# Performance work log

Hardware: AMD Instinct MI355X
Metric: run time of the kernel (lower is better)

Reference implementation:

```python
import jax, jax.numpy as jnp
import numpy as np

N, E, D, H, C, TD, MD = 50000, 500000, 128, 2, 64, 32, 64


def setup_inputs() -> dict:
    key = jax.random.key(0)
    ks = jax.random.split(key, 16)
    s = 0.05
    return {
        "x": jax.random.normal(ks[0], (N, D), jnp.float32),
        "edge_index": jax.random.randint(ks[1], (2, E), 0, N, dtype=jnp.int64),
        "edge_time": jax.random.randint(ks[2], (E,), 0, 86400, dtype=jnp.int64),
        "msg": jax.random.normal(ks[3], (E, MD), jnp.float32),
        "Wt": jax.random.normal(ks[4], (1, TD), jnp.float32) * s,
        "bt": jax.random.normal(ks[5], (TD,), jnp.float32) * s,
        "Wq": jax.random.normal(ks[6], (D, H * C), jnp.float32) * s,
        "bq": jax.random.normal(ks[7], (H * C,), jnp.float32) * s,
        "Wk": jax.random.normal(ks[8], (D, H * C), jnp.float32) * s,
        "bk": jax.random.normal(ks[9], (H * C,), jnp.float32) * s,
        "Wv": jax.random.normal(ks[10], (D, H * C), jnp.float32) * s,
        "bv": jax.random.normal(ks[11], (H * C,), jnp.float32) * s,
        "We": jax.random.normal(ks[12], (TD + MD, H * C), jnp.float32) * s,
        "Wskip": jax.random.normal(ks[13], (D, H * C), jnp.float32) * s,
        "bskip": jax.random.normal(ks[14], (H * C,), jnp.float32) * s,
    }


def reference(x, edge_index, edge_time, msg, Wt, bt, Wq, bq, Wk, bk, Wv, bv, We, Wskip, bskip):
    n = x.shape[0]
    src, dst = edge_index[0], edge_index[1]

    # TGN-style time encoding: cos(Linear(t))  -> [E, TD]
    t = edge_time.astype(x.dtype)[:, None]
    rel_t = jnp.cos(t @ Wt + bt)
    edge_attr = jnp.concatenate([rel_t, msg], axis=-1)  # [E, TD+MD]

    # TransformerConv projections, reshaped to [n, H, C] then gathered per edge
    q = (x @ Wq + bq).reshape(n, H, C)[dst]   # [E, H, C]
    k = (x @ Wk + bk).reshape(n, H, C)[src]   # [E, H, C]
    v = (x @ Wv + bv).reshape(n, H, C)[src]   # [E, H, C]
    e = (edge_attr @ We).reshape(-1, H, C)    # [E, H, C]

    k = k + e
    alpha = (q * k).sum(-1) / jnp.sqrt(jnp.asarray(C, x.dtype))  # [E, H]

    # segment softmax over incoming edges of each dst node
    amax = jax.ops.segment_max(alpha, dst, num_segments=n)       # [n, H]
    amax = jnp.where(jnp.isfinite(amax), amax, 0.0)
    ex = jnp.exp(alpha - amax[dst])
    denom = jax.ops.segment_sum(ex, dst, num_segments=n)
    alpha = ex / (denom[dst] + 1e-16)                            # [E, H]

    out_e = (v + e) * alpha[..., None]                           # [E, H, C]
    out = jax.ops.segment_sum(out_e, dst, num_segments=n).reshape(n, H * C)

    # root/skip connection
    out = out + x @ Wskip + bskip
    return out
```

## Files before the change

kernel.cpp:

```cpp
#include <hip/hip_runtime.h>
#include <hip/hip_bf16.h>

#define NN 50000
#define NE 500000
#define DD 128
#define HCC 128
#define TDD 32
#define MDD 64

typedef __hip_bfloat16 bf16;
typedef _Float16 f16;
typedef __attribute__((ext_vector_type(8))) _Float16 f16x8;
typedef __attribute__((ext_vector_type(2))) _Float16 f16x2;
typedef __attribute__((ext_vector_type(4))) float f32x4;

__device__ __forceinline__ float2 bf2x(unsigned u) {
    union { unsigned v; float f; } a, b;
    a.v = u << 16; b.v = u & 0xffff0000u;
    float2 r; r.x = a.f; r.y = b.f; return r;
}

__global__ __launch_bounds__(256) void conv_w_kernel(
    const float* __restrict__ Wq, const float* __restrict__ Wk,
    const float* __restrict__ Wv, const float* __restrict__ Wsk,
    const float* __restrict__ We,
    f16* __restrict__ WTh, f16* __restrict__ Weh, int* __restrict__ cnt)
{
    int idx = blockIdx.x * 256 + threadIdx.x;
    if (idx < 512 * 128) {
        int n = idx >> 7, k = idx & 127;
        int mat = n >> 7, col = n & 127;
        const float* W = (mat == 0) ? Wq : (mat == 1) ? Wk : (mat == 2) ? Wv : Wsk;
        WTh[idx] = (f16)W[k * 128 + col];
    } else if (idx < 512 * 128 + 96 * 128) {
        int i = idx - 512 * 128;
        Weh[i] = (f16)We[i];
    } else if (idx < 512 * 128 + 96 * 128 + NN) {
        cnt[idx - (512 * 128 + 96 * 128)] = 0;
    }
}

__global__ __launch_bounds__(256) void node_proj_kernel(
    const float* __restrict__ x, const f16* __restrict__ WTh,
    const float* __restrict__ bq, const float* __restrict__ bk,
    const float* __restrict__ bv, const float* __restrict__ bsk,
    f16* __restrict__ qh, f16* __restrict__ kh, f16* __restrict__ vh,
    float* __restrict__ outp)
{
    __shared__ f16 xs[64 * 136];
    __shared__ f16 ws[128 * 136];

    const int node0 = blockIdx.x * 64;
    const int g = blockIdx.y;

    for (int i = threadIdx.x; i < 64 * 32; i += 256) {
        int node = i >> 5, koff = (i & 31) * 4;
        int gn = node0 + node;
        f16 o4[4] = { (f16)0.f, (f16)0.f, (f16)0.f, (f16)0.f };
        if (gn < NN) {
            float4 v = *(const float4*)&x[(size_t)gn * DD + koff];
            o4[0] = (f16)v.x; o4[1] = (f16)v.y; o4[2] = (f16)v.z; o4[3] = (f16)v.w;
        }
        *(uint2*)&xs[node * 136 + koff] = *(uint2*)o4;
    }
    const f16* wt = WTh + (size_t)g * 128 * 128;
    for (int i = threadIdx.x; i < 128 * 32; i += 256) {
        int n = i >> 5, koff = (i & 31) * 4;
        *(uint2*)&ws[n * 136 + koff] = *(const uint2*)&wt[n * 128 + koff];
    }
    __syncthreads();

    const int wave = threadIdx.x >> 6;
    const int lane = threadIdx.x & 63;
    const int m0 = wave * 16;
    const int lrow = lane & 15;
    const int lk = (lane >> 4) * 8;

    f32x4 acc[8];
    #pragma unroll
    for (int t = 0; t < 8; t++) acc[t] = (f32x4){0.f, 0.f, 0.f, 0.f};

    #pragma unroll
    for (int kc = 0; kc < 4; kc++) {
        f16x8 a = *(const f16x8*)&xs[(m0 + lrow) * 136 + kc * 32 + lk];
        #pragma unroll
        for (int t = 0; t < 8; t++) {
            f16x8 b = *(const f16x8*)&ws[(t * 16 + lrow) * 136 + kc * 32 + lk];
            acc[t] = __builtin_amdgcn_mfma_f32_16x16x32_f16(a, b, acc[t], 0, 0, 0);
        }
    }

    const float* bias = (g == 0) ? bq : (g == 1) ? bk : (g == 2) ? bv : bsk;
    f16* outh = (g == 0) ? qh : (g == 1) ? kh : vh;

    #pragma unroll 1
    for (int t = 0; t < 8; t++) {
        int col = t * 16 + lrow;
        float bc = bias[col];
        #pragma unroll
        for (int r = 0; r < 4; r++) {
            int node = node0 + m0 + (lane >> 4) * 4 + r;
            if (node < NN) {
                float val = acc[t][r] + bc;
                if (g < 3) outh[(size_t)node * HCC + col] = (f16)val;
                else       outp[(size_t)node * HCC + col] = val;
            }
        }
    }
}

__global__ __launch_bounds__(256) void g_kernel(
    const f16* __restrict__ qh, const f16* __restrict__ Weh,
    bf16* __restrict__ G)
{
    __shared__ f16 qs[64 * 136];
    __shared__ f16 ws[96 * 136];

    const int node0 = blockIdx.x * 64;
    for (int i = threadIdx.x; i < 64 * 32; i += 256) {
        int node = i >> 5, koff = (i & 31) * 4;
        int gn = node0 + node;
        uint2 val = {0u, 0u};
        if (gn < NN) val = *(const uint2*)&qh[(size_t)gn * DD + koff];
        *(uint2*)&qs[node * 136 + koff] = val;
    }
    for (int i = threadIdx.x; i < 96 * 32; i += 256) {
        int j = i >> 5, koff = (i & 31) * 4;
        *(uint2*)&ws[j * 136 + koff] = *(const uint2*)&Weh[j * 128 + koff];
    }
    __syncthreads();

    const int wave = threadIdx.x >> 6;
    const int lane = threadIdx.x & 63;
    const int m0 = wave * 16;
    const int lrow = lane & 15;
    const int lk = (lane >> 4) * 8;

    f16x8 afr[4];
    #pragma unroll
    for (int hk = 0; hk < 4; hk++) {
        int h = hk >> 1, kc = hk & 1;
        afr[hk] = *(const f16x8*)&qs[(m0 + lrow) * 136 + h * 64 + kc * 32 + lk];
    }

    f32x4 acc[12];
    #pragma unroll
    for (int t = 0; t < 12; t++) acc[t] = (f32x4){0.f, 0.f, 0.f, 0.f};

    #pragma unroll
    for (int t = 0; t < 12; t++) {
        int h = (t < 6) ? 0 : 1;
        int jt = (t < 6) ? t : t - 6;
        #pragma unroll
        for (int kc = 0; kc < 2; kc++) {
            f16x8 b = *(const f16x8*)&ws[(jt * 16 + lrow) * 136 + h * 64 + kc * 32 + lk];
            acc[t] = __builtin_amdgcn_mfma_f32_16x16x32_f16(afr[h * 2 + kc], b, acc[t], 0, 0, 0);
        }
    }

    #pragma unroll 1
    for (int t = 0; t < 12; t++) {
        int h = (t < 6) ? 0 : 1;
        int jt = (t < 6) ? t : t - 6;
        int col = h * 96 + jt * 16 + lrow;
        #pragma unroll
        for (int r = 0; r < 4; r++) {
            int node = node0 + m0 + (lane >> 4) * 4 + r;
            if (node < NN) G[(size_t)node * 192 + col] = __float2bfloat16(acc[t][r]);
        }
    }
}

__global__ __launch_bounds__(256) void hist_kernel(
    const int* __restrict__ ei, int* __restrict__ cnt)
{
    int gid = blockIdx.x * 256 + threadIdx.x;
    if (gid < NE) atomicAdd(&cnt[ei[NE + gid]], 1);
}

__global__ __launch_bounds__(256) void scan_a_kernel(
    const int* __restrict__ cnt, int* __restrict__ bsum)
{
    __shared__ int red[256];
    int gid = blockIdx.x * 256 + threadIdx.x;
    red[threadIdx.x] = (gid < NN) ? cnt[gid] : 0;
    __syncthreads();
    for (int off = 128; off > 0; off >>= 1) {
        if (threadIdx.x < off) red[threadIdx.x] += red[threadIdx.x + off];
        __syncthreads();
    }
    if (threadIdx.x == 0) bsum[blockIdx.x] = red[0];
}

__global__ __launch_bounds__(256) void scan_b_kernel(
    const int* __restrict__ bsum, int* __restrict__ boff, int* __restrict__ seg)
{
    __shared__ int s[256];
    int t = threadIdx.x;
    s[t] = (t < 196) ? bsum[t] : 0;
    __syncthreads();
    if (t == 0) {
        int run = 0;
        for (int b = 0; b < 196; b++) { int v = s[b]; s[b] = run; run += v; }
        seg[NN] = NE;
    }
    __syncthreads();
    if (t < 196) boff[t] = s[t];
}

__global__ __launch_bounds__(256) void scan_c_kernel(
    const int* __restrict__ cnt, const int* __restrict__ boff,
    int* __restrict__ seg, int* __restrict__ cur)
{
    __shared__ int s[256];
    int gid = blockIdx.x * 256 + threadIdx.x;
    int v = (gid < NN) ? cnt[gid] : 0;
    s[threadIdx.x] = v;
    __syncthreads();
    for (int off = 1; off < 256; off <<= 1) {
        int t = (threadIdx.x >= off) ? s[threadIdx.x - off] : 0;
        __syncthreads();
        s[threadIdx.x] += t;
        __syncthreads();
    }
    int excl = s[threadIdx.x] - v + boff[blockIdx.x];
    if (gid < NN) { seg[gid] = excl; cur[gid] = excl; }
}

__global__ __launch_bounds__(256) void scatter_kernel(
    const int* __restrict__ ei, const int* __restrict__ et,
    int* __restrict__ cur, int4* __restrict__ epack)
{
    int gid = blockIdx.x * 256 + threadIdx.x;
    if (gid < NE) {
        int d = ei[NE + gid];
        int pos = atomicAdd(&cur[d], 1);
        int4 p;
        p.x = ei[gid];
        p.y = gid;
        p.z = __float_as_int((float)et[gid]);
        p.w = d;
        epack[pos] = p;
    }
}

__global__ __launch_bounds__(256) void agg_kernel(
    const int4* __restrict__ epack, const float* __restrict__ msg,
    const float* __restrict__ Wt, const float* __restrict__ bt,
    const f16* __restrict__ qh, const f16* __restrict__ kh,
    const f16* __restrict__ vh, const bf16* __restrict__ G,
    const int* __restrict__ seg,
    float* __restrict__ Sv, float* __restrict__ dnv,
    float* __restrict__ outp)
{
    __shared__ float wt_s[TDD], bt_s[TDD];
    if (threadIdx.x < TDD) {
        wt_s[threadIdx.x] = Wt[threadIdx.x];
        bt_s[threadIdx.x] = bt[threadIdx.x];
    }
    __syncthreads();

    const int lane = threadIdx.x & 63;
    const int c = lane & 31;
    const int h = lane >> 5;
    const float wtv = wt_s[c];
    const float btv = bt_s[c];
    const int gw = blockIdx.x * 4 + (threadIdx.x >> 6);
    const int NW = gridDim.x * 4;

    for (int n = gw; n < NN; n += NW) {
        const int s0 = seg[n], s1 = seg[n + 1];

        f16x2 q2 = *(const f16x2*)&qh[(size_t)n * DD + 2 * lane];
        const bf16* grow = G + (size_t)n * 192 + 96 * h;
        float Gc  = __bfloat162float(grow[c]);
        float Gm0 = __bfloat162float(grow[32 + 2 * c]);
        float Gm1 = __bfloat162float(grow[33 + 2 * c]);

        float2 acc; acc.x = 0.f; acc.y = 0.f;
        float accd = 0.f, sc = 0.f, sm0 = 0.f, sm1 = 0.f;

        int i = s0;
        #pragma unroll 1
        for (; i + 4 <= s1; i += 4) {
            int4 e[4]; f16x2 k2[4], v2[4]; float2 m[4];
            #pragma unroll
            for (int u = 0; u < 4; u++) e[u] = epack[i + u];
            #pragma unroll
            for (int u = 0; u < 4; u++) {
                int src = e[u].x;
                k2[u] = *(const f16x2*)&kh[(size_t)src * HCC + 2 * lane];
                v2[u] = *(const f16x2*)&vh[(size_t)src * HCC + 2 * lane];
                m[u]  = *(const float2*)&msg[((size_t)e[u].y << 6) + 2 * c];
            }
            #pragma unroll
            for (int u = 0; u < 4; u++) {
                float t = __int_as_float(e[u].z);
                float cs = __cosf(fmaf(t, wtv, btv));
                float p = fmaf(cs, Gc, fmaf(m[u].x, Gm0, m[u].y * Gm1));
#if defined(__has_builtin) && __has_builtin(__builtin_amdgcn_fdot2)
                p = __builtin_amdgcn_fdot2(q2, k2[u], p, false);
#else
                p = fmaf((float)q2[0], (float)k2[u][0], p);
                p = fmaf((float)q2[1], (float)k2[u][1], p);
#endif
                p += __shfl_xor(p, 1);
                p += __shfl_xor(p, 2);
                p += __shfl_xor(p, 4);
                p += __shfl_xor(p, 8);
                p += __shfl_xor(p, 16);
                float ex = __expf(p * 0.125f);
                acc.x = fmaf(ex, (float)v2[u][0], acc.x);
                acc.y = fmaf(ex, (float)v2[u][1], acc.y);
                accd += ex;
                sc  = fmaf(ex, cs, sc);
                sm0 = fmaf(ex, m[u].x, sm0);
                sm1 = fmaf(ex, m[u].y, sm1);
            }
        }
        #pragma unroll 1
        for (; i < s1; i++) {
            int4 e = epack[i];
            int src = e.x;
            f16x2 k2 = *(const f16x2*)&kh[(size_t)src * HCC + 2 * lane];
            f16x2 v2 = *(const f16x2*)&vh[(size_t)src * HCC + 2 * lane];
            float2 m = *(const float2*)&msg[((size_t)e.y << 6) + 2 * c];
            float t = __int_as_float(e.z);
            float cs = __cosf(fmaf(t, wtv, btv));
            float p = fmaf(cs, Gc, fmaf(m.x, Gm0, m.y * Gm1));
#if defined(__has_builtin) && __has_builtin(__builtin_amdgcn_fdot2)
            p = __builtin_amdgcn_fdot2(q2, k2, p, false);
#else
            p = fmaf((float)q2[0], (float)k2[0], p);
            p = fmaf((float)q2[1], (float)k2[1], p);
#endif
            p += __shfl_xor(p, 1);
            p += __shfl_xor(p, 2);
            p += __shfl_xor(p, 4);
            p += __shfl_xor(p, 8);
            p += __shfl_xor(p, 16);
            float ex = __expf(p * 0.125f);
            acc.x = fmaf(ex, (float)v2[0], acc.x);
            acc.y = fmaf(ex, (float)v2[1], acc.y);
            accd += ex;
            sc  = fmaf(ex, cs, sc);
            sm0 = fmaf(ex, m.x, sm0);
            sm1 = fmaf(ex, m.y, sm1);
        }

        float dn = accd + 1e-16f;
        size_t sb = (size_t)n * 192 + 96 * h;
        Sv[sb + c]          = sc;
        Sv[sb + 32 + 2 * c] = sm0;
        Sv[sb + 33 + 2 * c] = sm1;
        if (c == 0) dnv[n * 2 + h] = accd;

        size_t nb = (size_t)n * HCC + 2 * lane;
        float2 sk = *(const float2*)&outp[nb];
        float2 o;
        o.x = acc.x / dn + sk.x;
        o.y = acc.y / dn + sk.y;
        *(float2*)&outp[nb] = o;
    }
}

__global__ __launch_bounds__(256) void epi_kernel(
    const float* __restrict__ Sv, const float* __restrict__ dnv,
    const float* __restrict__ We, float* __restrict__ outp)
{
    __shared__ float st[192 * 36];
    const int node0 = blockIdx.x * 32;
    for (int idx = threadIdx.x; idx < 32 * 192; idx += 256) {
        int n = idx / 192, c = idx - n * 192;
        int node = node0 + n;
        st[c * 36 + n] = (node < NN) ? Sv[(size_t)node * 192 + c] : 0.f;
    }
    __syncthreads();

    const int wave = threadIdx.x >> 6;
    const int lane = threadIdx.x & 63;
    const int nb = wave * 8;
    const int hoff = (lane < 32) ? 0 : 96;
    const float2* We2 = (const float2*)We;

    float a[8][2];
    #pragma unroll
    for (int n = 0; n < 8; n++) { a[n][0] = 0.f; a[n][1] = 0.f; }

    #pragma unroll 8
    for (int j = 0; j < 96; j++) {
        float2 w = We2[j * 64 + lane];
        const float* sr = &st[(hoff + j) * 36 + nb];
        float sv[8];
        *(float4*)&sv[0] = *(const float4*)sr;
        *(float4*)&sv[4] = *(const float4*)(sr + 4);
        #pragma unroll
        for (int n = 0; n < 8; n++) {
            a[n][0] = fmaf(sv[n], w.x, a[n][0]);
            a[n][1] = fmaf(sv[n], w.y, a[n][1]);
        }
    }

    #pragma unroll 1
    for (int n = 0; n < 8; n++) {
        int node = node0 + nb + n;
        if (node >= NN) break;
        float dn = dnv[node * 2 + (lane >> 5)] + 1e-16f;
        size_t b = (size_t)node * HCC + 2 * lane;
        float2 o = *(const float2*)&outp[b];
        o.x += a[n][0] / dn;
        o.y += a[n][1] / dn;
        *(float2*)&outp[b] = o;
    }
}

extern "C" void kernel_launch(void* const* d_in, const int* in_sizes, int n_in,
                              void* d_out, int out_size, void* d_ws, size_t ws_size,
                              hipStream_t stream) {
    const float* x   = (const float*)d_in[0];
    const int* ei    = (const int*)d_in[1];
    const int* et    = (const int*)d_in[2];
    const float* msg = (const float*)d_in[3];
    const float* Wt  = (const float*)d_in[4];
    const float* bt  = (const float*)d_in[5];
    const float* Wq  = (const float*)d_in[6];
    const float* bq  = (const float*)d_in[7];
    const float* Wk  = (const float*)d_in[8];
    const float* bk  = (const float*)d_in[9];
    const float* Wv  = (const float*)d_in[10];
    const float* bv  = (const float*)d_in[11];
    const float* We  = (const float*)d_in[12];
    const float* Wsk = (const float*)d_in[13];
    const float* bsk = (const float*)d_in[14];

    const size_t nf = (size_t)NN * HCC;
    f16* qh      = (f16*)d_ws;
    f16* kh      = qh + nf;
    f16* vh      = kh + nf;
    f16* WTh     = vh + nf;
    f16* Weh     = WTh + 512 * 128;
    bf16* G      = (bf16*)(Weh + 96 * 128);
    float* Sv    = (float*)(G + (size_t)NN * 192);
    float* dnv   = Sv + (size_t)NN * 192;
    int4* epack  = (int4*)(dnv + (size_t)NN * 2);
    int* cnt     = (int*)(epack + NE);
    int* seg     = cnt + NN;
    int* cur     = seg + NN + 1;
    int* bsum    = cur + NN;
    int* boff    = bsum + 256;
    size_t need  = (size_t)((char*)(boff + 256) - (char*)d_ws);
    if (ws_size < need) return;

    float* outp = (float*)d_out;

    conv_w_kernel<<<(512 * 128 + 96 * 128 + NN + 255) / 256, 256, 0, stream>>>(
        Wq, Wk, Wv, Wsk, We, WTh, Weh, cnt);
    dim3 npgrid((NN + 63) / 64, 4);
    node_proj_kernel<<<npgrid, 256, 0, stream>>>(
        x, WTh, bq, bk, bv, bsk, qh, kh, vh, outp);
    g_kernel<<<(NN + 63) / 64, 256, 0, stream>>>(qh, Weh, G);
    hist_kernel<<<(NE + 255) / 256, 256, 0, stream>>>(ei, cnt);
    scan_a_kernel<<<196, 256, 0, stream>>>(cnt, bsum);
    scan_b_kernel<<<1, 256, 0, stream>>>(bsum, boff, seg);
    scan_c_kernel<<<196, 256, 0, stream>>>(cnt, boff, seg, cur);
    scatter_kernel<<<(NE + 255) / 256, 256, 0, stream>>>(ei, et, cur, epack);
    agg_kernel<<<3125, 256, 0, stream>>>(
        epack, msg, Wt, bt, qh, kh, vh, G, seg, Sv, dnv, outp);
    epi_kernel<<<(NN + 31) / 32, 256, 0, stream>>>(Sv, dnv, We, outp);
}
```

Measured before the change: 539.0 us.

## Interleave K/V per node and process two edges per wave in aggregation

Node projection now writes K and V into one interleaved buffer (4 K values then 4 V values per 8-element group), so each edge gathers K and V with a single 16-byte load. The aggregation kernel splits each wave into two 32-lane halves that handle alternate edges, with each lane covering 4 channels, and the halves are combined with cross-half shuffles at the end. The aim is fewer, wider gather loads and fewer shuffle reduction steps per edge. The tail path uses a predicated edge body that recomputes a dummy edge, and the final combination adds shuffle overhead per node.

```diff
diff --git a/kernel.cpp b/kernel.cpp
--- a/kernel.cpp
+++ b/kernel.cpp
@@ -19,6 +19,16 @@
     a.v = u << 16; b.v = u & 0xffff0000u;
     float2 r; r.x = a.f; r.y = b.f; return r;
 }
+
+#if defined(__has_builtin) && __has_builtin(__builtin_amdgcn_fdot2)
+#define FDOT2(a, b, acc) __builtin_amdgcn_fdot2((a), (b), (acc), false)
+#else
+__device__ __forceinline__ float fdot2_sw(f16x2 a, f16x2 b, float acc) {
+    acc = fmaf((float)a[0], (float)b[0], acc);
+    return fmaf((float)a[1], (float)b[1], acc);
+}
+#define FDOT2(a, b, acc) fdot2_sw((a), (b), (acc))
+#endif
 
 __global__ __launch_bounds__(256) void conv_w_kernel(
     const float* __restrict__ Wq, const float* __restrict__ Wk,
@@ -44,7 +54,7 @@
     const float* __restrict__ x, const f16* __restrict__ WTh,
     const float* __restrict__ bq, const float* __restrict__ bk,
     const float* __restrict__ bv, const float* __restrict__ bsk,
-    f16* __restrict__ qh, f16* __restrict__ kh, f16* __restrict__ vh,
+    f16* __restrict__ qh, f16* __restrict__ kvh,
     float* __restrict__ outp)
 {
     __shared__ f16 xs[64 * 136];
@@ -91,7 +101,6 @@
     }
 
     const float* bias = (g == 0) ? bq : (g == 1) ? bk : (g == 2) ? bv : bsk;
-    f16* outh = (g == 0) ? qh : (g == 1) ? kh : vh;
 
     #pragma unroll 1
     for (int t = 0; t < 8; t++) {
@@ -102,8 +111,12 @@
             int node = node0 + m0 + (lane >> 4) * 4 + r;
             if (node < NN) {
                 float val = acc[t][r] + bc;
-                if (g < 3) outh[(size_t)node * HCC + col] = (f16)val;
-                else       outp[(size_t)node * HCC + col] = val;
+                if (g == 0)      qh[(size_t)node * DD + col] = (f16)val;
+                else if (g == 3) outp[(size_t)node * HCC + col] = val;
+                else {
+                    int off = 8 * (col >> 2) + (col & 3) + ((g == 2) ? 4 : 0);
+                    kvh[(size_t)node * 256 + off] = (f16)val;
+                }
             }
         }
     }
@@ -247,120 +260,117 @@
 __global__ __launch_bounds__(256) void agg_kernel(
     const int4* __restrict__ epack, const float* __restrict__ msg,
     const float* __restrict__ Wt, const float* __restrict__ bt,
-    const f16* __restrict__ qh, const f16* __restrict__ kh,
-    const f16* __restrict__ vh, const bf16* __restrict__ G,
-    const int* __restrict__ seg,
+    const f16* __restrict__ qh, const f16* __restrict__ kvh,
+    const bf16* __restrict__ G, const int* __restrict__ seg,
     float* __restrict__ Sv, float* __restrict__ dnv,
     float* __restrict__ outp)
 {
-    __shared__ float wt_s[TDD], bt_s[TDD];
-    if (threadIdx.x < TDD) {
-        wt_s[threadIdx.x] = Wt[threadIdx.x];
-        bt_s[threadIdx.x] = bt[threadIdx.x];
-    }
-    __syncthreads();
-
     const int lane = threadIdx.x & 63;
-    const int c = lane & 31;
-    const int h = lane >> 5;
-    const float wtv = wt_s[c];
-    const float btv = bt_s[c];
+    const int l31 = lane & 31;
+    const int hl = (lane >> 4) & 1;
+    const int c = lane & 15;
+    const int halfid = lane >> 5;
+
+    const float wt0 = Wt[2 * c], wt1 = Wt[2 * c + 1];
+    const float bt0 = bt[2 * c], bt1 = bt[2 * c + 1];
+
     const int gw = blockIdx.x * 4 + (threadIdx.x >> 6);
     const int NW = gridDim.x * 4;
 
+    union QU { uint2 u; f16x2 h[2]; };
+    union KVU { uint4 u4; f16x2 h[4]; };
+
     for (int n = gw; n < NN; n += NW) {
         const int s0 = seg[n], s1 = seg[n + 1];
 
-        f16x2 q2 = *(const f16x2*)&qh[(size_t)n * DD + 2 * lane];
-        const bf16* grow = G + (size_t)n * 192 + 96 * h;
-        float Gc  = __bfloat162float(grow[c]);
-        float Gm0 = __bfloat162float(grow[32 + 2 * c]);
-        float Gm1 = __bfloat162float(grow[33 + 2 * c]);
-
-        float2 acc; acc.x = 0.f; acc.y = 0.f;
-        float accd = 0.f, sc = 0.f, sm0 = 0.f, sm1 = 0.f;
-
-        int i = s0;
-        #pragma unroll 1
-        for (; i + 4 <= s1; i += 4) {
-            int4 e[4]; f16x2 k2[4], v2[4]; float2 m[4];
-            #pragma unroll
-            for (int u = 0; u < 4; u++) e[u] = epack[i + u];
-            #pragma unroll
-            for (int u = 0; u < 4; u++) {
-                int src = e[u].x;
-                k2[u] = *(const f16x2*)&kh[(size_t)src * HCC + 2 * lane];
-                v2[u] = *(const f16x2*)&vh[(size_t)src * HCC + 2 * lane];
-                m[u]  = *(const float2*)&msg[((size_t)e[u].y << 6) + 2 * c];
-            }
-            #pragma unroll
-            for (int u = 0; u < 4; u++) {
-                float t = __int_as_float(e[u].z);
-                float cs = __cosf(fmaf(t, wtv, btv));
-                float p = fmaf(cs, Gc, fmaf(m[u].x, Gm0, m[u].y * Gm1));
-#if defined(__has_builtin) && __has_builtin(__builtin_amdgcn_fdot2)
-                p = __builtin_amdgcn_fdot2(q2, k2[u], p, false);
-#else
-                p = fmaf((float)q2[0], (float)k2[u][0], p);
-                p = fmaf((float)q2[1], (float)k2[u][1], p);
-#endif
-                p += __shfl_xor(p, 1);
-                p += __shfl_xor(p, 2);
-                p += __shfl_xor(p, 4);
-                p += __shfl_xor(p, 8);
-                p += __shfl_xor(p, 16);
-                float ex = __expf(p * 0.125f);
-                acc.x = fmaf(ex, (float)v2[u][0], acc.x);
-                acc.y = fmaf(ex, (float)v2[u][1], acc.y);
-                accd += ex;
-                sc  = fmaf(ex, cs, sc);
-                sm0 = fmaf(ex, m[u].x, sm0);
-                sm1 = fmaf(ex, m[u].y, sm1);
-            }
-        }
-        #pragma unroll 1
-        for (; i < s1; i++) {
-            int4 e = epack[i];
-            int src = e.x;
-            f16x2 k2 = *(const f16x2*)&kh[(size_t)src * HCC + 2 * lane];
-            f16x2 v2 = *(const f16x2*)&vh[(size_t)src * HCC + 2 * lane];
-            float2 m = *(const float2*)&msg[((size_t)e.y << 6) + 2 * c];
+        QU q; q.u = *(const uint2*)&qh[(size_t)n * DD + 4 * l31];
+        const bf16* grow = G + (size_t)n * 192 + 96 * hl;
+        const float Gc0 = __bfloat162float(grow[2 * c]);
+        const float Gc1 = __bfloat162float(grow[2 * c + 1]);
+        const float Gm0 = __bfloat162float(grow[32 + 4 * c]);
+        const float Gm1 = __bfloat162float(grow[33 + 4 * c]);
+        const float Gm2 = __bfloat162float(grow[34 + 4 * c]);
+        const float Gm3 = __bfloat162float(grow[35 + 4 * c]);
+
+        f32x4 av = (f32x4){0.f, 0.f, 0.f, 0.f};
+        f32x4 sm = (f32x4){0.f, 0.f, 0.f, 0.f};
+        float accd = 0.f, sc0 = 0.f, sc1 = 0.f;
+
+        auto edge_body = [&](int iu, bool pred) {
+            int ic = pred ? iu : s0;
+            int4 e = epack[ic];
+            KVU kv;
+            kv.u4 = *(const uint4*)&kvh[(size_t)e.x * 256 + 8 * l31];
+            float4 m = *(const float4*)&msg[((size_t)e.y << 6) + 4 * c];
             float t = __int_as_float(e.z);
-            float cs = __cosf(fmaf(t, wtv, btv));
-            float p = fmaf(cs, Gc, fmaf(m.x, Gm0, m.y * Gm1));
-#if defined(__has_builtin) && __has_builtin(__builtin_amdgcn_fdot2)
-            p = __builtin_amdgcn_fdot2(q2, k2, p, false);
-#else
-            p = fmaf((float)q2[0], (float)k2[0], p);
-            p = fmaf((float)q2[1], (float)k2[1], p);
-#endif
+            float cs0 = __cosf(fmaf(t, wt0, bt0));
+            float cs1 = __cosf(fmaf(t, wt1, bt1));
+            float p = fmaf(cs0, Gc0, cs1 * Gc1);
+            p = fmaf(m.x, Gm0, p); p = fmaf(m.y, Gm1, p);
+            p = fmaf(m.z, Gm2, p); p = fmaf(m.w, Gm3, p);
+            p = FDOT2(q.h[0], kv.h[0], p);
+            p = FDOT2(q.h[1], kv.h[1], p);
             p += __shfl_xor(p, 1);
             p += __shfl_xor(p, 2);
             p += __shfl_xor(p, 4);
             p += __shfl_xor(p, 8);
-            p += __shfl_xor(p, 16);
-            float ex = __expf(p * 0.125f);
-            acc.x = fmaf(ex, (float)v2[0], acc.x);
-            acc.y = fmaf(ex, (float)v2[1], acc.y);
+            float ex = pred ? __expf(p * 0.125f) : 0.f;
+            av.x = fmaf(ex, (float)kv.h[2][0], av.x);
+            av.y = fmaf(ex, (float)kv.h[2][1], av.y);
+            av.z = fmaf(ex, (float)kv.h[3][0], av.z);
+            av.w = fmaf(ex, (float)kv.h[3][1], av.w);
             accd += ex;
-            sc  = fmaf(ex, cs, sc);
-            sm0 = fmaf(ex, m.x, sm0);
-            sm1 = fmaf(ex, m.y, sm1);
-        }
-
-        float dn = accd + 1e-16f;
-        size_t sb = (size_t)n * 192 + 96 * h;
-        Sv[sb + c]          = sc;
-        Sv[sb + 32 + 2 * c] = sm0;
-        Sv[sb + 33 + 2 * c] = sm1;
-        if (c == 0) dnv[n * 2 + h] = accd;
-
-        size_t nb = (size_t)n * HCC + 2 * lane;
-        float2 sk = *(const float2*)&outp[nb];
-        float2 o;
-        o.x = acc.x / dn + sk.x;
-        o.y = acc.y / dn + sk.y;
-        *(float2*)&outp[nb] = o;
+            sc0 = fmaf(ex, cs0, sc0);
+            sc1 = fmaf(ex, cs1, sc1);
+            sm.x = fmaf(ex, m.x, sm.x);
+            sm.y = fmaf(ex, m.y, sm.y);
+            sm.z = fmaf(ex, m.z, sm.z);
+            sm.w = fmaf(ex, m.w, sm.w);
+        };
+
+        int ib = s0;
+        #pragma unroll 1
+        for (; ib + 8 <= s1; ib += 8) {
+            #pragma unroll
+            for (int u = 0; u < 4; u++)
+                edge_body(ib + 2 * u + halfid, true);
+        }
+        #pragma unroll 1
+        for (; ib < s1; ib += 2) {
+            int iu = ib + halfid;
+            edge_body(iu, iu < s1);
+        }
+
+        av.x += __shfl_xor(av.x, 32);
+        av.y += __shfl_xor(av.y, 32);
+        av.z += __shfl_xor(av.z, 32);
+        av.w += __shfl_xor(av.w, 32);
+        accd += __shfl_xor(accd, 32);
+        sc0  += __shfl_xor(sc0, 32);
+        sc1  += __shfl_xor(sc1, 32);
+        sm.x += __shfl_xor(sm.x, 32);
+        sm.y += __shfl_xor(sm.y, 32);
+        sm.z += __shfl_xor(sm.z, 32);
+        sm.w += __shfl_xor(sm.w, 32);
+
+        if (lane < 32) {
+            float dn = accd + 1e-16f;
+            size_t sb = (size_t)n * 192 + 96 * hl;
+            float2 scv; scv.x = sc0; scv.y = sc1;
+            *(float2*)&Sv[sb + 2 * c] = scv;
+            float4 smv; smv.x = sm.x; smv.y = sm.y; smv.z = sm.z; smv.w = sm.w;
+            *(float4*)&Sv[sb + 32 + 4 * c] = smv;
+            if (c == 0) dnv[2 * n + hl] = accd;
+
+            size_t nb = (size_t)n * HCC + 4 * l31;
+            float4 sk = *(const float4*)&outp[nb];
+            float4 o;
+            o.x = av.x / dn + sk.x;
+            o.y = av.y / dn + sk.y;
+            o.z = av.z / dn + sk.z;
+            o.w = av.w / dn + sk.w;
+            *(float4*)&outp[nb] = o;
+        }
     }
 }
 
@@ -435,9 +445,8 @@
 
     const size_t nf = (size_t)NN * HCC;
     f16* qh      = (f16*)d_ws;
-    f16* kh      = qh + nf;
-    f16* vh      = kh + nf;
-    f16* WTh     = vh + nf;
+    f16* kvh     = qh + nf;
+    f16* WTh     = kvh + 2 * nf;
     f16* Weh     = WTh + 512 * 128;
     bf16* G      = (bf16*)(Weh + 96 * 128);
     float* Sv    = (float*)(G + (size_t)NN * 192);
@@ -457,7 +466,7 @@
         Wq, Wk, Wv, Wsk, We, WTh, Weh, cnt);
     dim3 npgrid((NN + 63) / 64, 4);
     node_proj_kernel<<<npgrid, 256, 0, stream>>>(
-        x, WTh, bq, bk, bv, bsk, qh, kh, vh, outp);
+        x, WTh, bq, bk, bv, bsk, qh, kvh, outp);
     g_kernel<<<(NN + 63) / 64, 256, 0, stream>>>(qh, Weh, G);
     hist_kernel<<<(NE + 255) / 256, 256, 0, stream>>>(ei, cnt);
     scan_a_kernel<<<196, 256, 0, stream>>>(cnt, bsum);
@@ -465,6 +474,6 @@
     scan_c_kernel<<<196, 256, 0, stream>>>(cnt, boff, seg, cur);
     scatter_kernel<<<(NE + 255) / 256, 256, 0, stream>>>(ei, et, cur, epack);
     agg_kernel<<<3125, 256, 0, stream>>>(
-        epack, msg, Wt, bt, qh, kh, vh, G, seg, Sv, dnv, outp);
+        epack, msg, Wt, bt, qh, kvh, G, seg, Sv, dnv, outp);
     epi_kernel<<<(NN + 31) / 32, 256, 0, stream>>>(Sv, dnv, We, outp);
 }
```

After: 537.8 us. No clear change (-0.2%).
